# Performance work log

Hardware: AMD Instinct MI355X
Metric: run time of the kernel (lower is better)

Reference implementation:

```python
import jax, jax.numpy as jnp
import numpy as np

B, N, DIM = 2, 512, 256
H, DH = 8, 32
INNER = H * DH        # 256
EDGE_DIM = DIM        # default(edge_dim, dim)
SCALE = DH ** -0.5


def setup_inputs() -> dict:
    key = jax.random.key(0)
    ks = jax.random.split(key, 12)
    s = 0.02
    f32 = jnp.float32
    nodes = jax.random.normal(ks[0], (B, N, DIM), f32)
    edges = jax.random.normal(ks[1], (B, N, N, EDGE_DIM), f32)
    Wq  = jax.random.normal(ks[2], (DIM, INNER), f32) * s
    bq  = jax.random.normal(ks[3], (INNER,), f32) * s
    Wkv = jax.random.normal(ks[4], (DIM, 2 * INNER), f32) * s
    bkv = jax.random.normal(ks[5], (2 * INNER,), f32) * s
    We  = jax.random.normal(ks[6], (EDGE_DIM, INNER), f32) * s
    be  = jax.random.normal(ks[7], (INNER,), f32) * s
    Wo  = jax.random.normal(ks[8], (INNER, DIM), f32) * s
    bo  = jax.random.normal(ks[9], (DIM,), f32) * s
    return {"nodes": nodes, "edges": edges, "Wq": Wq, "bq": bq,
            "Wkv": Wkv, "bkv": bkv, "We": We, "be": be, "Wo": Wo, "bo": bo}


def reference(nodes, edges, Wq, bq, Wkv, bkv, We, be, Wo, bo):
    b, n, _ = nodes.shape
    # projections
    q = (nodes @ Wq + bq).reshape(b, n, H, DH).transpose(0, 2, 1, 3)   # b h i d
    kv = nodes @ Wkv + bkv
    k, v = jnp.split(kv, 2, axis=-1)
    k = k.reshape(b, n, H, DH).transpose(0, 2, 1, 3)                   # b h j d
    v = v.reshape(b, n, H, DH).transpose(0, 2, 1, 3)                   # b h j d
    e = (edges @ We + be).reshape(b, n, n, H, DH).transpose(0, 3, 1, 2, 4)  # b h i j d
    # sim = q . (k + e)  — split to avoid materializing k broadcast; same math
    sim = (jnp.einsum('bhid,bhjd->bhij', q, k)
           + jnp.einsum('bhid,bhijd->bhij', q, e)) * SCALE
    attn = jax.nn.softmax(sim, axis=-1)
    # out = attn . (v + e)
    out = (jnp.einsum('bhij,bhjd->bhid', attn, v)
           + jnp.einsum('bhij,bhijd->bhid', attn, e))
    out = out.transpose(0, 2, 1, 3).reshape(b, n, INNER)               # b n (h d)
    return out @ Wo + bo
```

## Files before the change

### kernel.cpp

```cpp
#include <hip/hip_runtime.h>
#include <hip/hip_bf16.h>
#include <stdint.h>

#define NB 2
#define NN 512
#define NDIM 256
#define NH 8
#define NDH 32
#define SCALE 0.17677669529663687f

__global__ __launch_bounds__(256) void k_proj(
    const float* __restrict__ nodes, const float* __restrict__ Wq, const float* __restrict__ bq,
    const float* __restrict__ Wkv, const float* __restrict__ bkv,
    const float* __restrict__ We, const float* __restrict__ be,
    float* __restrict__ q, float* __restrict__ k, float* __restrict__ v,
    float* __restrict__ qe, float* __restrict__ qbe)
{
    const int row = blockIdx.x;
    const int t = threadIdx.x;
    __shared__ float xs[NDIM];
    __shared__ float qs[NDIM];
    xs[t] = nodes[(size_t)row*NDIM + t];
    __syncthreads();

    float accq = bq[t];
    float acck = bkv[t];
    float accv = bkv[t + NDIM];
    #pragma unroll 4
    for (int d = 0; d < NDIM; ++d) {
        float x = xs[d];
        accq += x * Wq[(size_t)d*NDIM + t];
        acck += x * Wkv[(size_t)d*2*NDIM + t];
        accv += x * Wkv[(size_t)d*2*NDIM + t + NDIM];
    }
    q[(size_t)row*NDIM + t] = accq;
    k[(size_t)row*NDIM + t] = acck;
    v[(size_t)row*NDIM + t] = accv;
    qs[t] = accq;
    __syncthreads();

    float qacc[NH];
    #pragma unroll
    for (int h = 0; h < NH; ++h) qacc[h] = 0.f;
    const float* wrow = We + (size_t)t*NDIM;
    #pragma unroll
    for (int h = 0; h < NH; ++h) {
        float a0 = 0.f, a1 = 0.f, a2 = 0.f, a3 = 0.f;
        #pragma unroll
        for (int d4 = 0; d4 < NDH/4; ++d4) {
            float4 w4 = *(const float4*)(wrow + h*NDH + d4*4);
            const float* qp = qs + h*NDH + d4*4;
            a0 += qp[0]*w4.x; a1 += qp[1]*w4.y; a2 += qp[2]*w4.z; a3 += qp[3]*w4.w;
        }
        qacc[h] = (a0+a1)+(a2+a3);
    }
    #pragma unroll
    for (int h = 0; h < NH; ++h) qe[((size_t)row*NH + h)*NDIM + t] = qacc[h];
    if (t < NH) {
        float a = 0.f;
        #pragma unroll 4
        for (int d = 0; d < NDH; ++d) a += qs[t*NDH + d]*be[t*NDH + d];
        qbe[(size_t)row*NH + t] = a;
    }
}

__global__ __launch_bounds__(256) void k_attn(
    const float* __restrict__ edges,
    const float* __restrict__ We, const float* __restrict__ be,
    const float* __restrict__ Wo, const float* __restrict__ bo,
    const float* __restrict__ q, const float* __restrict__ k, const float* __restrict__ v,
    const float* __restrict__ qe, const float* __restrict__ qbe,
    float* __restrict__ out)
{
    const int row = blockIdx.x;
    const int b = row >> 9;
    const int t = threadIdx.x;
    const int gA = t & 31, sA = t >> 5;
    const int jlB = t & 31, hB = t >> 5;
    const int hC = t & 7,  cbC = t >> 3;
    const bool isv = (hC == (cbC >> 2));

    __shared__ float redbuf[32*293];
    __shared__ float pbuf[256];
    __shared__ float mh[8], lh[8], al[8];
    __shared__ float wfull[2048];
    __shared__ float ovfull[256];
    __shared__ float oibuf[256];

    float qe_r[8][8];
    {
        const float* qp = qe + ((size_t)row*NH)*NDIM + gA*8;
        #pragma unroll
        for (int h = 0; h < 8; ++h) {
            float4 a0 = *(const float4*)(qp + h*NDIM);
            float4 a1 = *(const float4*)(qp + h*NDIM + 4);
            qe_r[h][0]=a0.x; qe_r[h][1]=a0.y; qe_r[h][2]=a0.z; qe_r[h][3]=a0.w;
            qe_r[h][4]=a1.x; qe_r[h][5]=a1.y; qe_r[h][6]=a1.z; qe_r[h][7]=a1.w;
        }
    }
    const float qbeV = qbe[(size_t)row*NH + hB];
    float w_r[8], ov_r[8];
    #pragma unroll
    for (int r = 0; r < 8; ++r) { w_r[r] = 0.f; ov_r[r] = 0.f; }
    if (t < 8) { mh[t] = -1e30f; lh[t] = 0.f; }
    __syncthreads();

    const float* Erow = edges + (size_t)row*NN*NDIM;
    const float* qrow = q + (size_t)row*NDIM + hB*NDH;
    const float* krow = k + ((size_t)b*NN)*NDIM + hB*NDH;

    for (int jc = 0; jc < 16; ++jc) {
        const int j0 = jc*32;
        float4 ea[4], eb4[4];
        #pragma unroll
        for (int m = 0; m < 4; ++m) {
            const int jl = sA + m*8;
            const float* ep = Erow + (size_t)(j0+jl)*NDIM + gA*8;
            ea[m]  = *(const float4*)(ep);
            eb4[m] = *(const float4*)(ep + 4);
        }
        #pragma unroll
        for (int m = 0; m < 4; ++m) {
            const int jl = sA + m*8;
            float e[8];
            e[0]=ea[m].x; e[1]=ea[m].y; e[2]=ea[m].z; e[3]=ea[m].w;
            e[4]=eb4[m].x; e[5]=eb4[m].y; e[6]=eb4[m].z; e[7]=eb4[m].w;
            float sp[8];
            #pragma unroll
            for (int h = 0; h < 8; ++h) sp[h] = 0.f;
            #pragma unroll
            for (int c = 0; c < 8; ++c) {
                const float ec = e[c];
                #pragma unroll
                for (int h = 0; h < 8; ++h) sp[h] += qe_r[h][c]*ec;
            }
            float* rb = redbuf + jl*293 + gA*9;
            #pragma unroll
            for (int h = 0; h < 8; ++h) rb[h] = sp[h];
        }
        __syncthreads();
        {
            const int j = j0 + jlB;
            const float* kp = krow + (size_t)j*NDIM;
            float d0=0.f,d1=0.f,d2=0.f,d3=0.f;
            #pragma unroll
            for (int u = 0; u < 8; ++u) {
                float4 kv4 = *(const float4*)(kp + u*4);
                float4 qv4 = *(const float4*)(qrow + u*4);
                d0 += qv4.x*kv4.x; d1 += qv4.y*kv4.y;
                d2 += qv4.z*kv4.z; d3 += qv4.w*kv4.w;
            }
            const float* rb = redbuf + jlB*293 + hB;
            float r0=0.f,r1=0.f,r2=0.f,r3=0.f;
            #pragma unroll
            for (int g = 0; g < 32; g += 4) {
                r0 += rb[(g+0)*9]; r1 += rb[(g+1)*9];
                r2 += rb[(g+2)*9]; r3 += rb[(g+3)*9];
            }
            const float sim = SCALE*(((d0+d1)+(d2+d3)) + qbeV + ((r0+r1)+(r2+r3)));
            float cm = sim;
            #pragma unroll
            for (int off = 16; off >= 1; off >>= 1)
                cm = fmaxf(cm, __shfl_xor(cm, off, 64));
            const float mold = mh[hB];
            const float mnew = fmaxf(mold, cm);
            const float a_ = __expf(mold - mnew);
            const float p = __expf(sim - mnew);
            float ps = p;
            #pragma unroll
            for (int off = 16; off >= 1; off >>= 1)
                ps += __shfl_xor(ps, off, 64);
            if (jlB == 0) {
                mh[hB] = mnew;
                lh[hB] = lh[hB]*a_ + ps;
                al[hB] = a_;
            }
            pbuf[jlB*8 + hB] = p;
        }
        __syncthreads();
        {
            const float a_ = al[hC];
            #pragma unroll
            for (int r = 0; r < 8; ++r) w_r[r] *= a_;
            if (isv) {
                #pragma unroll
                for (int r = 0; r < 8; ++r) ov_r[r] *= a_;
            }
            const float* eb = Erow + (size_t)j0*NDIM + cbC*8;
            const float* vb = v + ((size_t)b*NN + j0)*NDIM + cbC*8;
            #pragma unroll 4
            for (int jl = 0; jl < 32; ++jl) {
                const float p = pbuf[jl*8 + hC];
                float4 e0 = *(const float4*)(eb + (size_t)jl*NDIM);
                float4 e1 = *(const float4*)(eb + (size_t)jl*NDIM + 4);
                w_r[0] += p*e0.x; w_r[1] += p*e0.y; w_r[2] += p*e0.z; w_r[3] += p*e0.w;
                w_r[4] += p*e1.x; w_r[5] += p*e1.y; w_r[6] += p*e1.z; w_r[7] += p*e1.w;
                if (isv) {
                    float4 v0 = *(const float4*)(vb + (size_t)jl*NDIM);
                    float4 v1 = *(const float4*)(vb + (size_t)jl*NDIM + 4);
                    ov_r[0] += p*v0.x; ov_r[1] += p*v0.y; ov_r[2] += p*v0.z; ov_r[3] += p*v0.w;
                    ov_r[4] += p*v1.x; ov_r[5] += p*v1.y; ov_r[6] += p*v1.z; ov_r[7] += p*v1.w;
                }
            }
        }
        __syncthreads();
    }

    #pragma unroll
    for (int r = 0; r < 8; ++r) wfull[hC*NDIM + cbC*8 + r] = w_r[r];
    if (isv) {
        #pragma unroll
        for (int r = 0; r < 8; ++r) ovfull[cbC*8 + r] = ov_r[r];
    }
    __syncthreads();
    {
        const int u = t, hu = u >> 5;
        const float linv = 1.f/lh[hu];
        const float* wrow = wfull + hu*NDIM;
        float a0=0.f,a1=0.f,a2=0.f,a3=0.f;
        #pragma unroll 2
        for (int c = 0; c < NDIM; c += 4) {
            a0 += wrow[c+0]*We[(size_t)(c+0)*NDIM + u];
            a1 += wrow[c+1]*We[(size_t)(c+1)*NDIM + u];
            a2 += wrow[c+2]*We[(size_t)(c+2)*NDIM + u];
            a3 += wrow[c+3]*We[(size_t)(c+3)*NDIM + u];
        }
        oibuf[u] = (ovfull[u] + ((a0+a1)+(a2+a3)))*linv + be[u];
    }
    __syncthreads();
    {
        const int u = t;
        float a0=bo[u],a1=0.f,a2=0.f,a3=0.f;
        #pragma unroll 2
        for (int x = 0; x < NDIM; x += 4) {
            a0 += oibuf[x+0]*Wo[(size_t)(x+0)*NDIM + u];
            a1 += oibuf[x+1]*Wo[(size_t)(x+1)*NDIM + u];
            a2 += oibuf[x+2]*Wo[(size_t)(x+2)*NDIM + u];
            a3 += oibuf[x+3]*Wo[(size_t)(x+3)*NDIM + u];
        }
        out[(size_t)row*NDIM + u] = (a0+a1)+(a2+a3);
    }
}

extern "C" void kernel_launch(void* const* d_in, const int* in_sizes, int n_in,
                              void* d_out, int out_size, void* d_ws, size_t ws_size,
                              hipStream_t stream) {
    const float* nodes = (const float*)d_in[0];
    const float* edges = (const float*)d_in[1];
    const float* Wq  = (const float*)d_in[2];
    const float* bq  = (const float*)d_in[3];
    const float* Wkv = (const float*)d_in[4];
    const float* bkv = (const float*)d_in[5];
    const float* We  = (const float*)d_in[6];
    const float* be  = (const float*)d_in[7];
    const float* Wo  = (const float*)d_in[8];
    const float* bo  = (const float*)d_in[9];
    (void)in_sizes; (void)n_in; (void)out_size; (void)ws_size;

    float* ws  = (float*)d_ws;
    float* q   = ws;
    float* k   = q  + 262144;
    float* v   = k  + 262144;
    float* qe  = v  + 262144;
    float* qbe = qe + 2097152;

    k_proj<<<dim3(NB*NN), dim3(256), 0, stream>>>(nodes, Wq, bq, Wkv, bkv, We, be,
                                                  q, k, v, qe, qbe);
    k_attn<<<dim3(NB*NN), dim3(256), 0, stream>>>(edges, We, be, Wo, bo,
                                                  q, k, v, qe, qbe,
                                                  (float*)d_out);
}
```

Before: 1.138 ms.

## Prefetch next edge chunk, reduce edge scores with shuffles, stage qe in LDS

Each block now loads the next 32-row edge chunk into registers while it processes the current one. The per-chunk q·e partial sums are reduced with a butterfly of cross-lane shuffles instead of a large padded shared-memory reduction buffer. The qe and q rows are staged in LDS rather than held in a 64-register array, and shared buffers are aliased into one union. A minimum of 4 blocks per CU is requested and the trailing per-chunk barrier is dropped. The aim is to hide global-load latency and to cut registers and LDS to raise occupancy. The cost is more shuffle traffic and LDS reads of qe in the inner loop.

After: 1.022 ms. -10.2%, faster.

```diff
diff --git a/kernel.cpp b/kernel.cpp
--- a/kernel.cpp
+++ b/kernel.cpp
@@ -64,7 +64,7 @@
     }
 }
 
-__global__ __launch_bounds__(256) void k_attn(
+__global__ __launch_bounds__(256, 4) void k_attn(
     const float* __restrict__ edges,
     const float* __restrict__ We, const float* __restrict__ be,
     const float* __restrict__ Wo, const float* __restrict__ bo,
@@ -80,84 +80,127 @@
     const int hC = t & 7,  cbC = t >> 3;
     const bool isv = (hC == (cbC >> 2));
 
-    __shared__ float redbuf[32*293];
-    __shared__ float pbuf[256];
+    __shared__ __align__(16) float uni[2560];
+    __shared__ __align__(16) float simbuf[32*9];
+    __shared__ __align__(16) float pbuf[256];
     __shared__ float mh[8], lh[8], al[8];
-    __shared__ float wfull[2048];
-    __shared__ float ovfull[256];
-    __shared__ float oibuf[256];
-
-    float qe_r[8][8];
+
+    float* qe_s   = uni;
+    float* qrow_s = uni + 2048;
+
+    const float* Erow = edges + (size_t)row*NN*NDIM;
+    const float* krow = k + (size_t)b*NN*NDIM + hB*NDH;
+
+    float4 ea[4], eb4[4];
     {
-        const float* qp = qe + ((size_t)row*NH)*NDIM + gA*8;
+        const float* ep0 = Erow + (size_t)sA*NDIM + gA*8;
+        #pragma unroll
+        for (int m = 0; m < 4; ++m) {
+            ea[m]  = *(const float4*)(ep0 + (size_t)m*8*NDIM);
+            eb4[m] = *(const float4*)(ep0 + (size_t)m*8*NDIM + 4);
+        }
+    }
+    {
+        const float* qp = qe + (size_t)row*(NH*NDIM) + t*8;
+        float4 a0 = *(const float4*)(qp);
+        float4 a1 = *(const float4*)(qp + 4);
+        *(float4*)(qe_s + t*8)     = a0;
+        *(float4*)(qe_s + t*8 + 4) = a1;
+        qrow_s[t] = q[(size_t)row*NDIM + t];
+    }
+    const float qbeV = qbe[(size_t)row*NH + hB];
+    float w_r[8], ov_r[8];
+    #pragma unroll
+    for (int r = 0; r < 8; ++r) { w_r[r] = 0.f; ov_r[r] = 0.f; }
+    if (t < 8) { mh[t] = -1e30f; lh[t] = 0.f; }
+    __syncthreads();
+
+    for (int jc = 0; jc < 16; ++jc) {
+        const int j0 = jc*32;
+        float v32_[32];
         #pragma unroll
         for (int h = 0; h < 8; ++h) {
-            float4 a0 = *(const float4*)(qp + h*NDIM);
-            float4 a1 = *(const float4*)(qp + h*NDIM + 4);
-            qe_r[h][0]=a0.x; qe_r[h][1]=a0.y; qe_r[h][2]=a0.z; qe_r[h][3]=a0.w;
-            qe_r[h][4]=a1.x; qe_r[h][5]=a1.y; qe_r[h][6]=a1.z; qe_r[h][7]=a1.w;
-        }
-    }
-    const float qbeV = qbe[(size_t)row*NH + hB];
-    float w_r[8], ov_r[8];
-    #pragma unroll
-    for (int r = 0; r < 8; ++r) { w_r[r] = 0.f; ov_r[r] = 0.f; }
-    if (t < 8) { mh[t] = -1e30f; lh[t] = 0.f; }
-    __syncthreads();
-
-    const float* Erow = edges + (size_t)row*NN*NDIM;
-    const float* qrow = q + (size_t)row*NDIM + hB*NDH;
-    const float* krow = k + ((size_t)b*NN)*NDIM + hB*NDH;
-
-    for (int jc = 0; jc < 16; ++jc) {
-        const int j0 = jc*32;
-        float4 ea[4], eb4[4];
-        #pragma unroll
-        for (int m = 0; m < 4; ++m) {
-            const int jl = sA + m*8;
-            const float* ep = Erow + (size_t)(j0+jl)*NDIM + gA*8;
-            ea[m]  = *(const float4*)(ep);
-            eb4[m] = *(const float4*)(ep + 4);
-        }
-        #pragma unroll
-        for (int m = 0; m < 4; ++m) {
-            const int jl = sA + m*8;
-            float e[8];
-            e[0]=ea[m].x; e[1]=ea[m].y; e[2]=ea[m].z; e[3]=ea[m].w;
-            e[4]=eb4[m].x; e[5]=eb4[m].y; e[6]=eb4[m].z; e[7]=eb4[m].w;
-            float sp[8];
-            #pragma unroll
-            for (int h = 0; h < 8; ++h) sp[h] = 0.f;
-            #pragma unroll
-            for (int c = 0; c < 8; ++c) {
-                const float ec = e[c];
-                #pragma unroll
-                for (int h = 0; h < 8; ++h) sp[h] += qe_r[h][c]*ec;
-            }
-            float* rb = redbuf + jl*293 + gA*9;
-            #pragma unroll
-            for (int h = 0; h < 8; ++h) rb[h] = sp[h];
-        }
+            const float4 qa = *(const float4*)(qe_s + h*NDIM + gA*8);
+            const float4 qb = *(const float4*)(qe_s + h*NDIM + gA*8 + 4);
+            #pragma unroll
+            for (int m = 0; m < 4; ++m) {
+                v32_[m*8+h] =
+                    ea[m].x*qa.x + ea[m].y*qa.y + ea[m].z*qa.z + ea[m].w*qa.w +
+                    eb4[m].x*qb.x + eb4[m].y*qb.y + eb4[m].z*qb.z + eb4[m].w*qb.w;
+            }
+        }
+        float v16_[16];
+        {
+            const bool bb = (gA & 16) != 0;
+            #pragma unroll
+            for (int i = 0; i < 16; ++i) {
+                const float lo = v32_[i], hi = v32_[i+16];
+                const float ot = __shfl_xor(bb ? lo : hi, 16, 64);
+                v16_[i] = (bb ? hi : lo) + ot;
+            }
+        }
+        float v8_[8];
+        {
+            const bool bb = (gA & 8) != 0;
+            #pragma unroll
+            for (int i = 0; i < 8; ++i) {
+                const float lo = v16_[i], hi = v16_[i+8];
+                const float ot = __shfl_xor(bb ? lo : hi, 8, 64);
+                v8_[i] = (bb ? hi : lo) + ot;
+            }
+        }
+        float v4_[4];
+        {
+            const bool bb = (gA & 4) != 0;
+            #pragma unroll
+            for (int i = 0; i < 4; ++i) {
+                const float lo = v8_[i], hi = v8_[i+4];
+                const float ot = __shfl_xor(bb ? lo : hi, 4, 64);
+                v4_[i] = (bb ? hi : lo) + ot;
+            }
+        }
+        float v2_[2];
+        {
+            const bool bb = (gA & 2) != 0;
+            #pragma unroll
+            for (int i = 0; i < 2; ++i) {
+                const float lo = v4_[i], hi = v4_[i+2];
+                const float ot = __shfl_xor(bb ? lo : hi, 2, 64);
+                v2_[i] = (bb ? hi : lo) + ot;
+            }
+        }
+        float sacc;
+        {
+            const bool bb = (gA & 1) != 0;
+            const float lo = v2_[0], hi = v2_[1];
+            const float ot = __shfl_xor(bb ? lo : hi, 1, 64);
+            sacc = (bb ? hi : lo) + ot;
+        }
+        simbuf[(sA + (gA >> 3)*8)*9 + (gA & 7)] = sacc;
         __syncthreads();
+
+        if (jc < 15) {
+            const float* epn = Erow + (size_t)(j0 + 32 + sA)*NDIM + gA*8;
+            #pragma unroll
+            for (int m = 0; m < 4; ++m) {
+                ea[m]  = *(const float4*)(epn + (size_t)m*8*NDIM);
+                eb4[m] = *(const float4*)(epn + (size_t)m*8*NDIM + 4);
+            }
+        }
+
         {
             const int j = j0 + jlB;
             const float* kp = krow + (size_t)j*NDIM;
+            const float* qp = qrow_s + hB*NDH;
             float d0=0.f,d1=0.f,d2=0.f,d3=0.f;
             #pragma unroll
             for (int u = 0; u < 8; ++u) {
                 float4 kv4 = *(const float4*)(kp + u*4);
-                float4 qv4 = *(const float4*)(qrow + u*4);
+                float4 qv4 = *(const float4*)(qp + u*4);
                 d0 += qv4.x*kv4.x; d1 += qv4.y*kv4.y;
                 d2 += qv4.z*kv4.z; d3 += qv4.w*kv4.w;
             }
-            const float* rb = redbuf + jlB*293 + hB;
-            float r0=0.f,r1=0.f,r2=0.f,r3=0.f;
-            #pragma unroll
-            for (int g = 0; g < 32; g += 4) {
-                r0 += rb[(g+0)*9]; r1 += rb[(g+1)*9];
-                r2 += rb[(g+2)*9]; r3 += rb[(g+3)*9];
-            }
-            const float sim = SCALE*(((d0+d1)+(d2+d3)) + qbeV + ((r0+r1)+(r2+r3)));
+            const float sim = SCALE*(((d0+d1)+(d2+d3)) + qbeV + simbuf[jlB*9 + hB]);
             float cm = sim;
             #pragma unroll
             for (int off = 16; off >= 1; off >>= 1)
@@ -203,9 +246,11 @@
                 }
             }
         }
-        __syncthreads();
-    }
-
+    }
+
+    float* wfull  = uni;
+    float* ovfull = uni + 2048;
+    float* oibuf  = uni + 2304;
     #pragma unroll
     for (int r = 0; r < 8; ++r) wfull[hC*NDIM + cbC*8 + r] = w_r[r];
     if (isv) {
```
